# Performance work log

Hardware: AMD Instinct MI355X
Metric: run time of the kernel (lower is better)

## Reference

```python
import jax, jax.numpy as jnp
import numpy as np

NUM_EMBEDDINGS = 1024
EMBEDDING_DIM = 256
COMMITMENT_COST = 0.25


def setup_inputs() -> dict:
    key = jax.random.key(0)
    k1, k2 = jax.random.split(key)
    x = jax.random.normal(k1, (32, EMBEDDING_DIM, 32, 32), dtype=jnp.float32)
    codebook = jax.random.uniform(
        k2, (NUM_EMBEDDINGS, EMBEDDING_DIM), dtype=jnp.float32,
        minval=-1.0 / NUM_EMBEDDINGS, maxval=1.0 / NUM_EMBEDDINGS)
    return {"x": x, "codebook": codebook}


def reference(x, codebook):
    # x: [B, C, H, W] -> [B, H, W, C]
    inputs = jnp.transpose(x, (0, 2, 3, 1))
    B, H, W, D = inputs.shape
    K = codebook.shape[0]
    flat = inputs.reshape(-1, D)  # [N, D]

    # squared L2 distances to each code: [N, K]
    distances = (jnp.sum(flat ** 2, axis=1, keepdims=True)
                 + jnp.sum(codebook ** 2, axis=1)
                 - 2.0 * flat @ codebook.T)
    idx = jnp.argmin(distances, axis=1)  # [N]

    # gather codes (equivalent to one-hot @ codebook, without materializing one-hot)
    quantized = codebook[idx].reshape(inputs.shape)

    e_latent_loss = jnp.mean((jax.lax.stop_gradient(quantized) - inputs) ** 2)
    q_latent_loss = jnp.mean((quantized - jax.lax.stop_gradient(inputs)) ** 2)
    loss = q_latent_loss + COMMITMENT_COST * e_latent_loss

    # straight-through estimator
    quantized_st = inputs + jax.lax.stop_gradient(quantized - inputs)

    # perplexity from code usage histogram (mean of one-hot encodings)
    N = flat.shape[0]
    avg_probs = jnp.zeros((K,), dtype=flat.dtype).at[idx].add(1.0) / N
    perplexity = jnp.exp(-jnp.sum(avg_probs * jnp.log(avg_probs + 1e-10)))

    out = jnp.transpose(quantized_st, (0, 3, 1, 2))  # back to [B, C, H, W]
    return (out, loss, perplexity)
```

## Files before the change

### kernel.cpp

```cpp
#include <hip/hip_runtime.h>
#include <hip/hip_fp16.h>

typedef _Float16 half8 __attribute__((ext_vector_type(8)));
typedef __attribute__((ext_vector_type(4))) float f32x4;

#define OUT_ELEMS 8388608


__global__ __launch_bounds__(256) void prep_kernel(const float* __restrict__ cb,
        unsigned short* __restrict__ chs, float* __restrict__ sq,
        int* __restrict__ counts, float* __restrict__ loss) {
    const int t = threadIdx.x;
    if (blockIdx.x == 0) {
        ((int4*)counts)[t] = make_int4(0, 0, 0, 0);
        if (t == 0) *loss = 0.f;
    }
    const int row = blockIdx.x * 16 + (t >> 4);
    const int d0 = (t & 15) * 16;
    const float* src = cb + row * 256 + d0;
    half8 h0, h1;
    float s = 0.f;
#pragma unroll
    for (int i = 0; i < 16; ++i) {
        const float v = src[i];
        s += v * v;
        const _Float16 h = (_Float16)(v * 1024.f);
        if (i < 8) h0[i] = h; else h1[i - 8] = h;
    }
    *(half8*)(chs + row * 256 + d0) = h0;
    *(half8*)(chs + row * 256 + d0 + 8) = h1;
#pragma unroll
    for (int off = 1; off < 16; off <<= 1) s += __shfl_xor(s, off);
    if ((t & 15) == 0) sq[row] = s;
}

__global__ __launch_bounds__(512, 2) void argmin_kernel(
    const float* __restrict__ x, const unsigned short* __restrict__ chs,
    const float* __restrict__ sq, int* __restrict__ codeG,
    int* __restrict__ counts, float* __restrict__ loss_accum)
{
    __shared__ unsigned short Bs[2][2][16][264];
    __shared__ float mv[2][128];
    __shared__ int   mk[2][128];
    __shared__ float xsqL[128];
    __shared__ float wsum[2];

    const int t = threadIdx.x;
    const int lane = t & 63;
    const int w  = t >> 6;
    const int wg = w >> 2;
    const int wl = w & 3;
    const int m = lane & 15;
    const int q = lane >> 4;
    const int kb = wg << 9;
    const int bid = blockIdx.x;
    const int batch = bid >> 3;
    const int rowb = wl * 32;
    const int hwb = (bid & 7) << 7;
    const float* xb = x + (size_t)batch * 262144 + hwb + rowb + m;

    const int g  = t >> 8;
    const int tt = t & 255;
    const int scode = tt >> 4;
    const int sk = tt & 15;
    {
        const unsigned short* src = chs + ((g << 9) + scode) * 256 + sk * 16;
        *(half8*)&Bs[0][g][scode][sk * 16]     = *(const half8*)src;
        *(half8*)&Bs[0][g][scode][sk * 16 + 8] = *(const half8*)(src + 8);
    }

    half8 Ah[2][8];
#pragma unroll
    for (int f = 0; f < 2; ++f) {
        float xs = 0.f;
#pragma unroll
        for (int ks = 0; ks < 8; ++ks) {
            half8 a;
#pragma unroll
            for (int j = 0; j < 8; ++j) {
                const float v = xb[f * 16 + ((size_t)(ks * 32 + q * 8 + j) << 10)];
                xs += v * v;
                a[j] = (_Float16)v;
            }
            Ah[f][ks] = a;
        }
        xs += __shfl_xor(xs, 16);
        xs += __shfl_xor(xs, 32);
        if (wg == 0 && q == 0) xsqL[rowb + f * 16 + m] = xs;
    }

    float bestv[2][4];
    int   bestk[2][4];
#pragma unroll
    for (int f = 0; f < 2; ++f)
#pragma unroll
        for (int r = 0; r < 4; ++r) { bestv[f][r] = 3.4e38f; bestk[f][r] = 0; }

    float sc2 = sq[kb + m];

    for (int s = 0; s < 32; ++s) {
        const int buf = s & 1;
        half8 n0, n1;
        float sc2n;
        if (s + 1 < 32) {
            const unsigned short* src = chs + ((g << 9) + (s + 1) * 16 + scode) * 256 + sk * 16;
            n0 = *(const half8*)src;
            n1 = *(const half8*)(src + 8);
            sc2n = sq[kb + (s + 1) * 16 + m];
        }
        __syncthreads();
        f32x4 a0 = {0.f, 0.f, 0.f, 0.f}, a1 = {0.f, 0.f, 0.f, 0.f};
#pragma unroll
        for (int ks = 0; ks < 8; ++ks) {
            const half8 b = *(const half8*)&Bs[buf][wg][m][ks * 32 + q * 8];
            a0 = __builtin_amdgcn_mfma_f32_16x16x32_f16(Ah[0][ks], b, a0, 0, 0, 0);
            a1 = __builtin_amdgcn_mfma_f32_16x16x32_f16(Ah[1][ks], b, a1, 0, 0, 0);
        }
        const int code = kb + s * 16 + m;
#pragma unroll
        for (int f = 0; f < 2; ++f) {
            const f32x4 a = f ? a1 : a0;
#pragma unroll
            for (int r = 0; r < 4; ++r) {
                const float d0 = fmaf(-0.001953125f, a[r], sc2);
                if (d0 < bestv[f][r]) { bestv[f][r] = d0; bestk[f][r] = code; }
            }
        }
        if (s + 1 < 32) {
            *(half8*)&Bs[buf ^ 1][g][scode][sk * 16]     = n0;
            *(half8*)&Bs[buf ^ 1][g][scode][sk * 16 + 8] = n1;
            sc2 = sc2n;
        }
    }

#pragma unroll
    for (int f = 0; f < 2; ++f)
#pragma unroll
        for (int r = 0; r < 4; ++r) {
            float v = bestv[f][r];
            int   k = bestk[f][r];
#pragma unroll
            for (int d = 1; d < 16; d <<= 1) {
                const float ov = __shfl_xor(v, d);
                const int   ok = __shfl_xor(k, d);
                if (ov < v || (ov == v && ok < k)) { v = ov; k = ok; }
            }
            if (m == 0) {
                const int row = rowb + f * 16 + q * 4 + r;
                mv[wg][row] = v;
                mk[wg][row] = k;
            }
        }
    __syncthreads();

    if (t < 128) {
        const float v0 = mv[0][t]; const int k0 = mk[0][t];
        const float v1 = mv[1][t]; const int k1 = mk[1][t];
        const int   k = (v1 < v0) ? k1 : k0;
        const float v = (v1 < v0) ? v1 : v0;
        codeG[bid * 128 + t] = k;
        atomicAdd(&counts[k], 1);
        float lp = xsqL[t] + v;
#pragma unroll
        for (int off = 32; off > 0; off >>= 1) lp += __shfl_down(lp, off);
        if ((t & 63) == 0) wsum[t >> 6] = lp;
    }
    __syncthreads();
    if (t == 0) atomicAdd(loss_accum, wsum[0] + wsum[1]);
}

__global__ __launch_bounds__(256) void gather_kernel(
    const float* __restrict__ cb, const int* __restrict__ codeG,
    const int* __restrict__ counts, const float* __restrict__ loss_accum,
    float* __restrict__ out)
{
    __shared__ float Q[64][257];
    __shared__ int codeL[64];
    __shared__ float wsum[4];
    const int t = threadIdx.x;
    const int bid = blockIdx.x;
    if (t < 64) codeL[t] = codeG[bid * 64 + t];
    __syncthreads();
    {
        const int r = t & 63, seg = t >> 6;
        const float* src = cb + (size_t)codeL[r] * 256 + seg * 64;
#pragma unroll
        for (int i = 0; i < 16; ++i)
            *(float4*)&Q[r][seg * 64 + i * 4] = *(const float4*)(src + i * 4);
    }
    __syncthreads();
    const int batch = bid >> 4;
    const int hw0 = (bid & 15) << 6;
    const int hw4 = (t & 15) * 4;
    const int c0 = t >> 4;
    float* dst = out + (size_t)batch * 262144 + hw0 + hw4;
#pragma unroll
    for (int i = 0; i < 16; ++i) {
        const int c = c0 + i * 16;
        float4 v;
        v.x = Q[hw4 + 0][c];
        v.y = Q[hw4 + 1][c];
        v.z = Q[hw4 + 2][c];
        v.w = Q[hw4 + 3][c];
        *(float4*)(dst + (size_t)c * 1024) = v;
    }
    if (bid == 0) {
        float s = 0.f;
#pragma unroll
        for (int mm = 0; mm < 4; ++mm) {
            const float p = (float)counts[t + 256 * mm] * (1.f / 32768.f);
            s += p * logf(p + 1e-10f);
        }
#pragma unroll
        for (int off = 32; off > 0; off >>= 1) s += __shfl_down(s, off);
        if ((t & 63) == 0) wsum[t >> 6] = s;
        __syncthreads();
        if (t == 0) {
            out[OUT_ELEMS]     = loss_accum[0] * (1.25f / 8388608.f);
            out[OUT_ELEMS + 1] = expf(-(wsum[0] + wsum[1] + wsum[2] + wsum[3]));
        }
    }
}

extern "C" void kernel_launch(void* const* d_in, const int* in_sizes, int n_in,
                              void* d_out, int out_size, void* d_ws, size_t ws_size,
                              hipStream_t stream) {
    const float* x  = (const float*)d_in[0];
    const float* cb = (const float*)d_in[1];
    float* out = (float*)d_out;
    char* wsb = (char*)d_ws;
    int*            counts = (int*)(wsb + 0);
    float*          loss   = (float*)(wsb + 4096);
    float*          sq     = (float*)(wsb + 8192);
    unsigned short* chs    = (unsigned short*)(wsb + 16384);
    int*            codeG  = (int*)(wsb + 540672);

    prep_kernel<<<64, 256, 0, stream>>>(cb, chs, sq, counts, loss);
    argmin_kernel<<<256, 512, 0, stream>>>(x, chs, sq, codeG, counts, loss);
    gather_kernel<<<512, 256, 0, stream>>>(cb, codeG, counts, loss, out);
}
```

Before: 121.8 us.

## Use async global-to-LDS codebook loads with swizzled layout and 64-row warp tiles

The codebook fp16 copy is now stored in a pre-tiled, XOR-swizzled layout so each block can stream 32KB stages straight into LDS with global_load_lds, instead of staging through registers. The warp split changes from 2 code groups × 4 row groups to 4 code groups × 2 row groups, so each warp holds 64 rows of A and issues 4 MFMAs per B fragment. This cuts the register round-trip and LDS bank conflicts and raises B reuse. In exchange it uses more registers for A fragments and accumulators, doubles LDS per block, and needs a wider final cross-group reduction.

```diff
diff --git a/kernel.cpp b/kernel.cpp
--- a/kernel.cpp
+++ b/kernel.cpp
@@ -27,8 +27,11 @@
         const _Float16 h = (_Float16)(v * 1024.f);
         if (i < 8) h0[i] = h; else h1[i - 8] = h;
     }
-    *(half8*)(chs + row * 256 + d0) = h0;
-    *(half8*)(chs + row * 256 + d0 + 8) = h1;
+    const int g = row >> 8, sidx = (row >> 4) & 15, m = row & 15, e = m & 7;
+    const int j0 = (t & 15) * 2;
+    unsigned short* tile = chs + sidx * 16384 + g * 4096 + m * 256;
+    *(half8*)(tile + (((j0    ) ^ e) << 3)) = h0;
+    *(half8*)(tile + (((j0 + 1) ^ e) << 3)) = h1;
 #pragma unroll
     for (int off = 1; off < 16; off <<= 1) s += __shfl_xor(s, off);
     if ((t & 15) == 0) sq[row] = s;
@@ -39,39 +42,43 @@
     const float* __restrict__ sq, int* __restrict__ codeG,
     int* __restrict__ counts, float* __restrict__ loss_accum)
 {
-    __shared__ unsigned short Bs[2][2][16][264];
-    __shared__ float mv[2][128];
-    __shared__ int   mk[2][128];
+    __shared__ __align__(16) unsigned char Bs[2][32768];
+    __shared__ float mv[4][128];
+    __shared__ int   mk[4][128];
     __shared__ float xsqL[128];
     __shared__ float wsum[2];
 
     const int t = threadIdx.x;
     const int lane = t & 63;
     const int w  = t >> 6;
-    const int wg = w >> 2;
-    const int wl = w & 3;
+    const int wg = w >> 1;
+    const int wl = w & 1;
     const int m = lane & 15;
     const int q = lane >> 4;
-    const int kb = wg << 9;
+    const int kb = wg << 8;
     const int bid = blockIdx.x;
     const int batch = bid >> 3;
-    const int rowb = wl * 32;
+    const int rowb = wl << 6;
     const int hwb = (bid & 7) << 7;
     const float* xb = x + (size_t)batch * 262144 + hwb + rowb + m;
 
-    const int g  = t >> 8;
-    const int tt = t & 255;
-    const int scode = tt >> 4;
-    const int sk = tt & 15;
+    const char* chsB = (const char*)chs;
+    char* bsB = (char*)&Bs[0][0];
+    const int stoff = w * 4096 + lane * 16;
+
     {
-        const unsigned short* src = chs + ((g << 9) + scode) * 256 + sk * 16;
-        *(half8*)&Bs[0][g][scode][sk * 16]     = *(const half8*)src;
-        *(half8*)&Bs[0][g][scode][sk * 16 + 8] = *(const half8*)(src + 8);
-    }
-
-    half8 Ah[2][8];
-#pragma unroll
-    for (int f = 0; f < 2; ++f) {
+        const char* src = chsB + stoff;
+        char* dst = bsB + w * 4096;
+#pragma unroll
+        for (int i = 0; i < 4; ++i)
+            __builtin_amdgcn_global_load_lds(
+                (const __attribute__((address_space(1))) void*)(src + i * 1024),
+                (__attribute__((address_space(3))) void*)(dst + i * 1024), 16, 0, 0);
+    }
+
+    half8 Ah[4][8];
+#pragma unroll
+    for (int f = 0; f < 4; ++f) {
         float xs = 0.f;
 #pragma unroll
         for (int ks = 0; ks < 8; ++ks) {
@@ -89,52 +96,59 @@
         if (wg == 0 && q == 0) xsqL[rowb + f * 16 + m] = xs;
     }
 
-    float bestv[2][4];
-    int   bestk[2][4];
-#pragma unroll
-    for (int f = 0; f < 2; ++f)
+    float bestv[4][4];
+    int   bestk[4][4];
+#pragma unroll
+    for (int f = 0; f < 4; ++f)
 #pragma unroll
         for (int r = 0; r < 4; ++r) { bestv[f][r] = 3.4e38f; bestk[f][r] = 0; }
 
     float sc2 = sq[kb + m];
 
-    for (int s = 0; s < 32; ++s) {
+    const int rbase = wg * 8192 + m * 512 + ((q ^ (m & 3)) << 4);
+    const int eh = (m >> 2) & 1;
+
+    for (int s = 0; s < 16; ++s) {
         const int buf = s & 1;
-        half8 n0, n1;
-        float sc2n;
-        if (s + 1 < 32) {
-            const unsigned short* src = chs + ((g << 9) + (s + 1) * 16 + scode) * 256 + sk * 16;
-            n0 = *(const half8*)src;
-            n1 = *(const half8*)(src + 8);
-            sc2n = sq[kb + (s + 1) * 16 + m];
-        }
         __syncthreads();
-        f32x4 a0 = {0.f, 0.f, 0.f, 0.f}, a1 = {0.f, 0.f, 0.f, 0.f};
+        if (s + 1 < 16) {
+            const char* src = chsB + (s + 1) * 32768 + stoff;
+            char* dst = bsB + (buf ^ 1) * 32768 + w * 4096;
+#pragma unroll
+            for (int i = 0; i < 4; ++i)
+                __builtin_amdgcn_global_load_lds(
+                    (const __attribute__((address_space(1))) void*)(src + i * 1024),
+                    (__attribute__((address_space(3))) void*)(dst + i * 1024), 16, 0, 0);
+        }
+        float sc2n = 0.f;
+        if (s + 1 < 16) sc2n = sq[kb + (s + 1) * 16 + m];
+
+        f32x4 a0 = {0.f,0.f,0.f,0.f}, a1 = {0.f,0.f,0.f,0.f};
+        f32x4 a2 = {0.f,0.f,0.f,0.f}, a3 = {0.f,0.f,0.f,0.f};
+        const char* bp = bsB + buf * 32768 + rbase;
 #pragma unroll
         for (int ks = 0; ks < 8; ++ks) {
-            const half8 b = *(const half8*)&Bs[buf][wg][m][ks * 32 + q * 8];
+            const half8 b = *(const half8*)(bp + ((ks ^ eh) << 6));
             a0 = __builtin_amdgcn_mfma_f32_16x16x32_f16(Ah[0][ks], b, a0, 0, 0, 0);
             a1 = __builtin_amdgcn_mfma_f32_16x16x32_f16(Ah[1][ks], b, a1, 0, 0, 0);
+            a2 = __builtin_amdgcn_mfma_f32_16x16x32_f16(Ah[2][ks], b, a2, 0, 0, 0);
+            a3 = __builtin_amdgcn_mfma_f32_16x16x32_f16(Ah[3][ks], b, a3, 0, 0, 0);
         }
         const int code = kb + s * 16 + m;
 #pragma unroll
-        for (int f = 0; f < 2; ++f) {
-            const f32x4 a = f ? a1 : a0;
+        for (int f = 0; f < 4; ++f) {
+            const f32x4 a = (f == 0) ? a0 : (f == 1) ? a1 : (f == 2) ? a2 : a3;
 #pragma unroll
             for (int r = 0; r < 4; ++r) {
-                const float d0 = fmaf(-0.001953125f, a[r], sc2);
-                if (d0 < bestv[f][r]) { bestv[f][r] = d0; bestk[f][r] = code; }
-            }
-        }
-        if (s + 1 < 32) {
-            *(half8*)&Bs[buf ^ 1][g][scode][sk * 16]     = n0;
-            *(half8*)&Bs[buf ^ 1][g][scode][sk * 16 + 8] = n1;
-            sc2 = sc2n;
-        }
-    }
-
-#pragma unroll
-    for (int f = 0; f < 2; ++f)
+                const float d0v = fmaf(-0.001953125f, a[r], sc2);
+                if (d0v < bestv[f][r]) { bestv[f][r] = d0v; bestk[f][r] = code; }
+            }
+        }
+        sc2 = sc2n;
+    }
+
+#pragma unroll
+    for (int f = 0; f < 4; ++f)
 #pragma unroll
         for (int r = 0; r < 4; ++r) {
             float v = bestv[f][r];
@@ -154,10 +168,13 @@
     __syncthreads();
 
     if (t < 128) {
-        const float v0 = mv[0][t]; const int k0 = mk[0][t];
-        const float v1 = mv[1][t]; const int k1 = mk[1][t];
-        const int   k = (v1 < v0) ? k1 : k0;
-        const float v = (v1 < v0) ? v1 : v0;
+        float v = mv[0][t]; int k = mk[0][t];
+#pragma unroll
+        for (int g2 = 1; g2 < 4; ++g2) {
+            const float vg = mv[g2][t];
+            const int   kg = mk[g2][t];
+            if (vg < v) { v = vg; k = kg; }
+        }
         codeG[bid * 128 + t] = k;
         atomicAdd(&counts[k], 1);
         float lp = xsqL[t] + v;
```

After: 131.3 us. +7.8%, slower.
